# Optimization experiments

Hardware: AMD Instinct MI355X
Metric: run time of the kernel (lower is better)

## Reference

```python
import jax, jax.numpy as jnp
import numpy as np

T, C, H, E, TOPK = 8192, 1024, 4096, 8, 2
ALPHA = 0.01


def setup_inputs() -> dict:
    key = jax.random.key(0)
    ks = jax.random.split(key, 10)
    std = 0.01
    return {
        "x": jax.random.normal(ks[0], (T, C), dtype=jnp.float32),
        "gate_w": jax.random.normal(ks[1], (E, C), dtype=jnp.float32) * std,  # nn.init.normal_(std=0.01)
        "wg": jax.random.normal(ks[2], (E, C, H), dtype=jnp.float32) * 0.02,
        "wu": jax.random.normal(ks[3], (E, C, H), dtype=jnp.float32) * 0.02,
        "wd": jax.random.normal(ks[4], (E, H, C), dtype=jnp.float32) * 0.02,
        "swg": jax.random.normal(ks[5], (C, H), dtype=jnp.float32) * 0.02,
        "swu": jax.random.normal(ks[6], (C, H), dtype=jnp.float32) * 0.02,
        "swd": jax.random.normal(ks[7], (H, C), dtype=jnp.float32) * 0.02,
        "shared_scale": jnp.ones((1,), dtype=jnp.float32) * 0.5,
    }


def _swiglu(h, g, u, d):
    # SwiGLU FFN: W_down( silu(W_gate x) * W_up x )
    return (jax.nn.silu(h @ g) * (h @ u)) @ d


def reference(x, gate_w, wg, wu, wd, swg, swu, swd, shared_scale):
    # ---- gate (top-k softmax routing) ----
    logits = x @ gate_w.T                       # [T, E]
    scores = jax.nn.softmax(logits, axis=-1)    # [T, E]
    topk_w, topk_idx = jax.lax.top_k(scores, TOPK)
    topk_w = topk_w / jnp.sum(topk_w, axis=-1, keepdims=True)

    # per-token combine weight for each expert: sum_k w_k * [idx_k == e]  -> [T, E]
    comb = jnp.zeros((x.shape[0], E), dtype=x.dtype)
    comb = comb.at[jnp.arange(x.shape[0])[:, None], topk_idx].add(topk_w)

    # ---- routed experts (dispatch-FFN-combine, expressed as masked dense combine) ----
    y = jnp.zeros_like(x)
    for e in range(E):  # fixed small expert count
        y = y + comb[:, e:e + 1] * _swiglu(x, wg[e], wu[e], wd[e])

    # ---- shared expert ----
    y = y + shared_scale * _swiglu(x, swg, swu, swd)

    # ---- load-balancing aux loss (training mode) ----
    onehot = jax.nn.one_hot(topk_idx.reshape(-1), E, dtype=x.dtype)  # [T*K, E]
    ce = onehot.mean(axis=0)
    fi = ce * E
    Pi = scores.mean(axis=0)
    aux_loss = jnp.sum(Pi * fi) * ALPHA
    return y, aux_loss
```

## Files before the change

kernel.cpp:

```cpp
#include <hip/hip_runtime.h>
#include <hip/hip_bf16.h>
#include <stdint.h>

#define T_TOK 8192
#define CDIM  1024
#define HDIM  4096
#define NEXP  8
#define TOPK_ 2
#define GT_MAX 72
#define UT_MAX 104
#define GROWS_MAX (GT_MAX * 256)

typedef __attribute__((ext_vector_type(8))) short short8;
typedef __attribute__((ext_vector_type(4))) float f32x4;

__device__ __forceinline__ void gload16(const short* g, short* l) {
  __builtin_amdgcn_global_load_lds(
      (const __attribute__((address_space(1))) unsigned int*)(g),
      (__attribute__((address_space(3))) unsigned int*)(l), 16, 0, 0);
}

__global__ __launch_bounds__(256) void gate_kernel(
    const float* __restrict__ x, const float* __restrict__ gw,
    int* __restrict__ tokinfo, float* __restrict__ tokw,
    int* __restrict__ bcnt, float* __restrict__ spart,
    __hip_bfloat16* __restrict__ xb)
{
  const int wid = threadIdx.x >> 6, lane = threadIdx.x & 63;
  const int t = blockIdx.x * 4 + wid;
  float acc[NEXP];
#pragma unroll
  for (int e = 0; e < NEXP; ++e) acc[e] = 0.f;
  const float4* xr = (const float4*)x + (size_t)t * (CDIM / 4);
  const float4* gw4 = (const float4*)gw;
  uint2* xbo = (uint2*)(xb + (size_t)t * CDIM);
#pragma unroll
  for (int i = 0; i < CDIM / 256; ++i) {
    const float4 xv = xr[lane + 64 * i];
    union { __hip_bfloat16 h[4]; uint2 u; } o;
    o.h[0] = __float2bfloat16(xv.x); o.h[1] = __float2bfloat16(xv.y);
    o.h[2] = __float2bfloat16(xv.z); o.h[3] = __float2bfloat16(xv.w);
    xbo[lane + 64 * i] = o.u;
#pragma unroll
    for (int e = 0; e < NEXP; ++e) {
      const float4 gv = gw4[e * (CDIM / 4) + lane + 64 * i];
      acc[e] += xv.x * gv.x + xv.y * gv.y + xv.z * gv.z + xv.w * gv.w;
    }
  }
#pragma unroll
  for (int off = 32; off > 0; off >>= 1) {
#pragma unroll
    for (int e = 0; e < NEXP; ++e) acc[e] += __shfl_xor(acc[e], off);
  }
  float mx = acc[0];
#pragma unroll
  for (int e = 1; e < NEXP; ++e) mx = fmaxf(mx, acc[e]);
  float p[NEXP]; float s = 0.f;
#pragma unroll
  for (int e = 0; e < NEXP; ++e) { p[e] = __expf(acc[e] - mx); s += p[e]; }
  const float inv = 1.f / s;
#pragma unroll
  for (int e = 0; e < NEXP; ++e) p[e] *= inv;
  float v0 = p[0]; int i0 = 0;
#pragma unroll
  for (int e = 1; e < NEXP; ++e) if (p[e] > v0) { v0 = p[e]; i0 = e; }
  float v1 = -1.f; int i1 = 0;
#pragma unroll
  for (int e = 0; e < NEXP; ++e) if (e != i0 && p[e] > v1) { v1 = p[e]; i1 = e; }

  __shared__ float sp[4][NEXP];
  __shared__ int   se[4][2];
  __shared__ float swt[4][2];
  if (lane == 0) {
#pragma unroll
    for (int e = 0; e < NEXP; ++e) sp[wid][e] = p[e];
    const float wn = 1.f / (v0 + v1);
    se[wid][0] = i0; se[wid][1] = i1;
    swt[wid][0] = v0 * wn; swt[wid][1] = v1 * wn;
  }
  __syncthreads();
  if (threadIdx.x == 0) {
    int cnt[NEXP];
#pragma unroll
    for (int e = 0; e < NEXP; ++e) cnt[e] = 0;
#pragma unroll
    for (int tt = 0; tt < 4; ++tt) {
      const int e0 = se[tt][0], e1 = se[tt][1];
      const int r0 = cnt[e0]++; const int r1 = cnt[e1]++;
      tokinfo[blockIdx.x * 4 + tt] = e0 | (e1 << 3) | (r0 << 6) | (r1 << 10);
      ((float2*)tokw)[blockIdx.x * 4 + tt] = make_float2(swt[tt][0], swt[tt][1]);
    }
#pragma unroll
    for (int e = 0; e < NEXP; ++e) bcnt[blockIdx.x * NEXP + e] = cnt[e];
  }
  if (threadIdx.x < NEXP)
    spart[blockIdx.x * NEXP + threadIdx.x] =
        sp[0][threadIdx.x] + sp[1][threadIdx.x] + sp[2][threadIdx.x] + sp[3][threadIdx.x];
}

__global__ __launch_bounds__(512) void scan_kernel(
    const int* __restrict__ bcnt, int* __restrict__ boff, int* __restrict__ ecnt,
    const float* __restrict__ spart, float* __restrict__ aux_out,
    int* __restrict__ pad_off, int* __restrict__ tile_map, int* __restrict__ ntiles)
{
  const int w = threadIdx.x >> 6, l = threadIdx.x & 63;
  int run = 0;
#pragma unroll 4
  for (int c = 0; c < (T_TOK / 4) / 64; ++c) {
    const int b = c * 64 + l;
    const int v = bcnt[b * NEXP + w];
    int sc = v;
#pragma unroll
    for (int off = 1; off < 64; off <<= 1) {
      const int t = __shfl_up(sc, off);
      if (l >= off) sc += t;
    }
    boff[b * NEXP + w] = run + sc - v;
    run += __shfl(sc, 63);
  }
  if (l == 0) ecnt[w] = run;
  float fs = 0.f;
  for (int c = 0; c < (T_TOK / 4) / 64; ++c) fs += spart[(c * 64 + l) * NEXP + w];
#pragma unroll
  for (int off = 32; off > 0; off >>= 1) fs += __shfl_xor(fs, off);
  __shared__ float pis[NEXP];
  __shared__ int cs[NEXP];
  if (l == 0) { pis[w] = fs; cs[w] = run; }
  __syncthreads();
  if (threadIdx.x == 0) {
    float aux = 0.f;
#pragma unroll
    for (int e = 0; e < NEXP; ++e) {
      const float Pi = pis[e] / (float)T_TOK;
      const float ce = (float)cs[e] / (float)(T_TOK * TOPK_);
      aux += Pi * ce * (float)NEXP;
    }
    aux_out[0] = aux * 0.01f;
    ecnt[8] = T_TOK;
    int acc = 0, nt = 0;
    for (int e = 0; e < NEXP; ++e) {
      pad_off[e] = acc;
      const int te = (cs[e] + 255) >> 8;
      for (int t = 0; t < te; ++t) { tile_map[nt] = e | ((t * 256) << 4); ++nt; }
      acc += te * 256;
    }
    ntiles[0] = nt;
    for (int t = 0; t < T_TOK / 256; ++t) { tile_map[nt] = 8 | ((t * 256) << 4); ++nt; }
    ntiles[1] = nt;
  }
}

__global__ __launch_bounds__(256) void scatter_kernel(
    const int* __restrict__ tokinfo, const float* __restrict__ tokw,
    const int* __restrict__ boff, const int* __restrict__ pad_off,
    int* __restrict__ grows, float* __restrict__ gww, int2* __restrict__ tokpos)
{
  const int t = blockIdx.x * 256 + threadIdx.x;
  const int info = tokinfo[t];
  const int e0 = info & 7, e1 = (info >> 3) & 7;
  const int r0 = (info >> 6) & 15, r1 = (info >> 10) & 15;
  const int b = t >> 2;
  const float2 wv = ((const float2*)tokw)[t];
  const int g0 = pad_off[e0] + boff[b * NEXP + e0] + r0;
  grows[g0] = t; gww[g0] = wv.x;
  const int g1 = pad_off[e1] + boff[b * NEXP + e1] + r1;
  grows[g1] = t; gww[g1] = wv.y;
  tokpos[t] = make_int2(g0, g1);
}

struct TD { const float* src; __hip_bfloat16* dst; int N; int nsh; int M; };
struct TB { TD d[27]; };
__global__ __launch_bounds__(256) void tbatch_kernel(TB tb)
{
  const int m = blockIdx.x >> 12;
  const int t = blockIdx.x & 4095;
  const TD td = tb.d[m];
  const int n0 = (t & ((1 << td.nsh) - 1)) << 5;
  const int m0 = (t >> td.nsh) << 5;
  __shared__ float tile[32][33];
  const int tx = threadIdx.x & 31, ty = threadIdx.x >> 5;
#pragma unroll
  for (int i = 0; i < 4; ++i)
    tile[ty + 8 * i][tx] = td.src[(size_t)(m0 + ty + 8 * i) * td.N + n0 + tx];
  __syncthreads();
#pragma unroll
  for (int i = 0; i < 4; ++i)
    td.dst[(size_t)(n0 + ty + 8 * i) * td.M + m0 + tx] = __float2bfloat16(tile[tx][ty + 8 * i]);
}

__global__ __launch_bounds__(1024, 4) void gemm1_pipe_kernel(
    const __hip_bfloat16* __restrict__ Abase,
    const __hip_bfloat16* __restrict__ B0mat, const __hip_bfloat16* __restrict__ B1mat,
    __hip_bfloat16* __restrict__ midout,
    const int* __restrict__ rowlist, const int* __restrict__ ecnt,
    const int* __restrict__ tile_map, const int* __restrict__ ntiles,
    int mode, int tile_base)
{
  constexpr int K = CDIM;
  constexpr int NTL = K / 64;
  __shared__ __align__(16) short lds[65536];

  int ti = (int)blockIdx.y + tile_base;
  if (mode == 2) ti += ntiles[0];
  const int hi = (mode == 1) ? ntiles[0] : ntiles[1];
  if (ti >= hi) return;
  const int tm = tile_map[ti];
  const int e = tm & 15, rb = tm >> 4;
  const int rows_valid = ecnt[e] - rb;
  const int gbmid = (int)blockIdx.y * 256;
  const int glist = ti * 256;

  const int t = threadIdx.x, l = t & 63, w = t >> 6;
  const int wr = w >> 2, wc = w & 3;
  const int n0h = (int)blockIdx.x * 128;

  const int srow = t >> 3;
  const int ksrc = ((t & 7) ^ ((t >> 3) & 7)) * 8;
  const short* pA[2]; const short* pB[2];
#pragma unroll
  for (int j = 0; j < 2; ++j) {
    const int rl_ = j * 128 + srow;
    int rg;
    if (e == 8) rg = rb + rl_;
    else { const int c = rl_ < rows_valid ? rl_ : rows_valid - 1; rg = rowlist[glist + c]; }
    pA[j] = (const short*)Abase + (size_t)rg * K + ksrc;
    const int s = (rl_ >> 4) & 1;
    const int h = n0h + (rl_ >> 5) * 16 + (rl_ & 15);
    pB[j] = (const short*)(s ? B1mat : B0mat) + (size_t)e * CDIM * HDIM + (size_t)h * K + ksrc;
  }
  const int dst0 = t * 8;

#define STG(tt) { const int b_ = ((tt) & 1) * 16384; \
    gload16(pA[0] + (tt) * 64, lds + b_ + dst0); \
    gload16(pA[1] + (tt) * 64, lds + b_ + 8192 + dst0); \
    gload16(pB[0] + (tt) * 64, lds + 32768 + b_ + dst0); \
    gload16(pB[1] + (tt) * 64, lds + 32768 + b_ + 8192 + dst0); }

  const int l15 = l & 15;
  const int j0 = ((l >> 4) ^ (l & 7)) * 8;
  const int j1 = ((4 + (l >> 4)) ^ (l & 7)) * 8;
  const int arow = (wr * 64 + l15) * 64;
  const int brow = (wc * 64 + l15) * 64;

  f32x4 acc[4][4];
#pragma unroll
  for (int i = 0; i < 4; ++i)
#pragma unroll
    for (int j = 0; j < 4; ++j) acc[i][j] = (f32x4){0.f, 0.f, 0.f, 0.f};

  short8 af[4], bf[4];

  STG(0)
  for (int tt = 0; tt < NTL; ++tt) {
    asm volatile("s_waitcnt vmcnt(0)\n\ts_barrier" ::: "memory");
    __builtin_amdgcn_sched_barrier(0);
    if (tt + 1 < NTL) STG(tt + 1)
    const int ab = (tt & 1) * 16384, bb = 32768 + (tt & 1) * 16384;
#pragma unroll
    for (int ks = 0; ks < 2; ++ks) {
      const int cj = ks ? j1 : j0;
#pragma unroll
      for (int mi = 0; mi < 4; ++mi) af[mi] = *(const short8*)(lds + ab + arow + mi * 1024 + cj);
#pragma unroll
      for (int ni = 0; ni < 4; ++ni) bf[ni] = *(const short8*)(lds + bb + brow + ni * 1024 + cj);
      __builtin_amdgcn_s_setprio(1);
#pragma unroll
      for (int mi = 0; mi < 4; ++mi)
#pragma unroll
        for (int ni = 0; ni < 4; ++ni)
          acc[mi][ni] = __builtin_amdgcn_mfma_f32_16x16x32_bf16(af[mi], bf[ni], acc[mi][ni], 0, 0, 0);
      __builtin_amdgcn_s_setprio(0);
    }
  }
#undef STG

  const int rl = (l >> 4) * 4, cl = l & 15;
#pragma unroll
  for (int mi = 0; mi < 4; ++mi) {
#pragma unroll
    for (int j = 0; j < 4; ++j) {
      const int rlocal = wr * 64 + mi * 16 + rl + j;
      if (rlocal < rows_valid) {
        __hip_bfloat16* mp = midout + (size_t)(gbmid + rlocal) * HDIM;
#pragma unroll
        for (int jj = 0; jj < 2; ++jj) {
          const float g = acc[mi][jj * 2][j], u = acc[mi][jj * 2 + 1][j];
          const float sv = g / (1.f + __expf(-g));
          mp[n0h + wc * 32 + jj * 16 + cl] = __float2bfloat16(sv * u);
        }
      }
    }
  }
}

template <int OST>
__global__ __launch_bounds__(1024, 4) void gemm2_pipe_kernel(
    const __hip_bfloat16* __restrict__ mid, const __hip_bfloat16* __restrict__ wd9,
    float* __restrict__ mid2, float* __restrict__ y,
    const int* __restrict__ rowlist, const float* __restrict__ roww,
    const int* __restrict__ ecnt, const int* __restrict__ tile_map,
    const int* __restrict__ ntiles, const float* __restrict__ ssc,
    int mode, int tile_base)
{
  constexpr int K = HDIM;
  constexpr int NTL = K / 64;
  __shared__ __align__(16) short lds[49152];

  int ti = (int)blockIdx.y + tile_base;
  if (mode == 2) ti += ntiles[0];
  const int hi = (mode == 1) ? ntiles[0] : ntiles[1];
  if (ti >= hi) return;
  const int tm = tile_map[ti];
  const int e = tm & 15, rb = tm >> 4;
  const int rows_valid = ecnt[e] - rb;
  const int gbmid = (int)blockIdx.y * 256;
  const int glist = ti * 256;

  const int t = threadIdx.x, l = t & 63, w = t >> 6;
  const int wr = w >> 2, wc = w & 3;
  const int n0 = (int)blockIdx.x * 128;

  const int srow = t >> 3;
  const int ksrc = ((t & 7) ^ ((t >> 3) & 7)) * 8;
  const short* pA[2];
#pragma unroll
  for (int j = 0; j < 2; ++j)
    pA[j] = (const short*)mid + (size_t)(gbmid + j * 128 + srow) * K + ksrc;
  const short* pB0 = (const short*)wd9 + (size_t)e * CDIM * HDIM + (size_t)(n0 + srow) * K + ksrc;
  const int dst0 = t * 8;

#define STG2(tt) { const int a_ = ((tt) & 1) * 16384, b_ = 32768 + ((tt) & 1) * 8192; \
    gload16(pA[0] + (size_t)(tt) * 64, lds + a_ + dst0); \
    gload16(pA[1] + (size_t)(tt) * 64, lds + a_ + 8192 + dst0); \
    gload16(pB0   + (size_t)(tt) * 64, lds + b_ + dst0); }

  const int l15 = l & 15;
  const int j0 = ((l >> 4) ^ (l & 7)) * 8;
  const int j1 = ((4 + (l >> 4)) ^ (l & 7)) * 8;
  const int arow = (wr * 64 + l15) * 64;
  const int brow = (wc * 32 + l15) * 64;

  f32x4 acc[4][2];
#pragma unroll
  for (int i = 0; i < 4; ++i) { acc[i][0] = (f32x4){0.f,0.f,0.f,0.f}; acc[i][1] = (f32x4){0.f,0.f,0.f,0.f}; }

  short8 af[4], bf[2];

  STG2(0)
  for (int tt = 0; tt < NTL; ++tt) {
    asm volatile("s_waitcnt vmcnt(0)\n\ts_barrier" ::: "memory");
    __builtin_amdgcn_sched_barrier(0);
    if (tt + 1 < NTL) STG2(tt + 1)
    const int ab = (tt & 1) * 16384, bb = 32768 + (tt & 1) * 8192;
#pragma unroll
    for (int ks = 0; ks < 2; ++ks) {
      const int cj = ks ? j1 : j0;
#pragma unroll
      for (int mi = 0; mi < 4; ++mi) af[mi] = *(const short8*)(lds + ab + arow + mi * 1024 + cj);
      bf[0] = *(const short8*)(lds + bb + brow + cj);
      bf[1] = *(const short8*)(lds + bb + brow + 1024 + cj);
      __builtin_amdgcn_s_setprio(1);
#pragma unroll
      for (int mi = 0; mi < 4; ++mi) {
        acc[mi][0] = __builtin_amdgcn_mfma_f32_16x16x32_bf16(af[mi], bf[0], acc[mi][0], 0, 0, 0);
        acc[mi][1] = __builtin_amdgcn_mfma_f32_16x16x32_bf16(af[mi], bf[1], acc[mi][1], 0, 0, 0);
      }
      __builtin_amdgcn_s_setprio(0);
    }
  }
#undef STG2

  const int rl = (l >> 4) * 4, cl = l & 15;
  if (OST) {
#pragma unroll
    for (int mi = 0; mi < 4; ++mi) {
#pragma unroll
      for (int j = 0; j < 4; ++j) {
        const int rlocal = wr * 64 + mi * 16 + rl + j;
        if (rlocal < rows_valid) {
          float* mp = mid2 + (size_t)(glist + rlocal) * CDIM + n0 + wc * 32 + cl;
          mp[0]  = acc[mi][0][j];
          mp[16] = acc[mi][1][j];
        }
      }
    }
  } else {
    const float ss = ssc[0];
#pragma unroll
    for (int mi = 0; mi < 4; ++mi) {
#pragma unroll
      for (int j = 0; j < 4; ++j) {
        const int rlocal = wr * 64 + mi * 16 + rl + j;
        if (rlocal < rows_valid) {
          int tok; float wgt;
          if (e == 8) { tok = rb + rlocal; wgt = ss; }
          else { tok = rowlist[glist + rlocal]; wgt = roww[glist + rlocal]; }
          float* yp = y + (size_t)tok * CDIM + n0 + wc * 32 + cl;
          unsafeAtomicAdd(yp,      wgt * acc[mi][0][j]);
          unsafeAtomicAdd(yp + 16, wgt * acc[mi][1][j]);
        }
      }
    }
  }
}

__global__ __launch_bounds__(256) void combine_kernel(
    const float* __restrict__ mid2, const int* __restrict__ ntiles,
    const int2* __restrict__ tokpos, const float* __restrict__ tokw,
    const float* __restrict__ ssc, float* __restrict__ y)
{
  const int t = blockIdx.x;
  const int c = threadIdx.x * 4;
  const int dbase = ntiles[0] * 256;
  const int2 gp = tokpos[t];
  const float2 wv = ((const float2*)tokw)[t];
  const float ss = ssc[0];
  const float4 d = *(const float4*)(mid2 + (size_t)(dbase + t) * CDIM + c);
  const float4 a = *(const float4*)(mid2 + (size_t)gp.x * CDIM + c);
  const float4 b = *(const float4*)(mid2 + (size_t)gp.y * CDIM + c);
  float4 r;
  r.x = ss * d.x + wv.x * a.x + wv.y * b.x;
  r.y = ss * d.y + wv.x * a.y + wv.y * b.y;
  r.z = ss * d.z + wv.x * a.z + wv.y * b.z;
  r.w = ss * d.w + wv.x * a.w + wv.y * b.w;
  *(float4*)(y + (size_t)t * CDIM + c) = r;
}

extern "C" void kernel_launch(void* const* d_in, const int* in_sizes, int n_in,
                              void* d_out, int out_size, void* d_ws, size_t ws_size,
                              hipStream_t stream)
{
  const float* x   = (const float*)d_in[0];
  const float* gw  = (const float*)d_in[1];
  const float* wg  = (const float*)d_in[2];
  const float* wu  = (const float*)d_in[3];
  const float* wd  = (const float*)d_in[4];
  const float* swg = (const float*)d_in[5];
  const float* swu = (const float*)d_in[6];
  const float* swd = (const float*)d_in[7];
  const float* ssc = (const float*)d_in[8];
  float* y = (float*)d_out;

  auto al = [](size_t v) { return (v + 255) & ~(size_t)255; };
  char* ws = (char*)d_ws;
  size_t off = 0;
  __hip_bfloat16* xb = (__hip_bfloat16*)(ws + off); off += al((size_t)T_TOK * CDIM * 2);
  int*   tokinfo = (int*)(ws + off);   off += al((size_t)T_TOK * 4);
  float* tokw    = (float*)(ws + off); off += al((size_t)T_TOK * 8);
  int2*  tokpos  = (int2*)(ws + off);  off += al((size_t)T_TOK * 8);
  int*   bcnt    = (int*)(ws + off);   off += al((size_t)(T_TOK / 4) * NEXP * 4);
  int*   boffb   = (int*)(ws + off);   off += al((size_t)(T_TOK / 4) * NEXP * 4);
  float* spart   = (float*)(ws + off); off += al((size_t)(T_TOK / 4) * NEXP * 4);
  int*   ecnt    = (int*)(ws + off);   off += 256;
  int*   pad_off = (int*)(ws + off);   off += 256;
  int*   ntiles  = (int*)(ws + off);   off += 256;
  int*   tile_map= (int*)(ws + off);   off += al((size_t)UT_MAX * 4);
  int*   grows   = (int*)(ws + off);   off += al((size_t)GROWS_MAX * 4);
  float* gww     = (float*)(ws + off); off += al((size_t)GROWS_MAX * 4);

  const size_t WMAT = (size_t)CDIM * HDIM;
  __hip_bfloat16* wg9 = (__hip_bfloat16*)(ws + off); off += 9 * WMAT * 2;
  __hip_bfloat16* wu9 = (__hip_bfloat16*)(ws + off); off += 9 * WMAT * 2;
  __hip_bfloat16* wd9 = (__hip_bfloat16*)(ws + off); off += 9 * WMAT * 2;
  __hip_bfloat16* mid = (__hip_bfloat16*)(ws + off);
  const size_t mid_avail = (ws_size > off) ? (ws_size - off) : 0;
  const size_t TILE_B = (size_t)256 * HDIM * 2;
  const size_t MIDB   = (size_t)UT_MAX * TILE_B;
  const size_t MID2B  = (size_t)UT_MAX * 256 * CDIM * 4;

  gate_kernel<<<T_TOK / 4, 256, 0, stream>>>(x, gw, tokinfo, tokw, bcnt, spart, xb);
  scan_kernel<<<1, 512, 0, stream>>>(bcnt, boffb, ecnt, spart, y + (size_t)T_TOK * CDIM,
                                     pad_off, tile_map, ntiles);
  scatter_kernel<<<T_TOK / 256, 256, 0, stream>>>(tokinfo, tokw, boffb, pad_off,
                                                  grows, gww, tokpos);

  TB tb;
  for (int e = 0; e < 8; ++e) {
    tb.d[e]      = TD{wg + e * WMAT, wg9 + e * WMAT, HDIM, 7, CDIM};
    tb.d[8 + e]  = TD{wu + e * WMAT, wu9 + e * WMAT, HDIM, 7, CDIM};
    tb.d[16 + e] = TD{wd + e * WMAT, wd9 + e * WMAT, CDIM, 5, HDIM};
  }
  tb.d[24] = TD{swg, wg9 + 8 * WMAT, HDIM, 7, CDIM};
  tb.d[25] = TD{swu, wu9 + 8 * WMAT, HDIM, 7, CDIM};
  tb.d[26] = TD{swd, wd9 + 8 * WMAT, CDIM, 5, HDIM};
  tbatch_kernel<<<27 * 4096, 256, 0, stream>>>(tb);

  if (mid_avail >= MIDB + MID2B) {
    float* mid2 = (float*)((char*)mid + MIDB);
    gemm1_pipe_kernel<<<dim3(HDIM / 128, UT_MAX), 1024, 0, stream>>>(
        xb, wg9, wu9, mid, grows, ecnt, tile_map, ntiles, 0, 0);
    gemm2_pipe_kernel<1><<<dim3(CDIM / 128, UT_MAX), 1024, 0, stream>>>(
        mid, wd9, mid2, nullptr, grows, gww, ecnt, tile_map, ntiles, ssc, 0, 0);
    combine_kernel<<<T_TOK, 256, 0, stream>>>(mid2, ntiles, tokpos, tokw, ssc, y);
  } else if (mid_avail >= MIDB) {
    hipMemsetAsync(y, 0, (size_t)T_TOK * CDIM * sizeof(float), stream);
    gemm1_pipe_kernel<<<dim3(HDIM / 128, UT_MAX), 1024, 0, stream>>>(
        xb, wg9, wu9, mid, grows, ecnt, tile_map, ntiles, 0, 0);
    gemm2_pipe_kernel<0><<<dim3(CDIM / 128, UT_MAX), 1024, 0, stream>>>(
        mid, wd9, nullptr, y, grows, gww, ecnt, tile_map, ntiles, ssc, 0, 0);
  } else {
    hipMemsetAsync(y, 0, (size_t)T_TOK * CDIM * sizeof(float), stream);
    int CH = (int)(mid_avail / TILE_B);
    if (CH < 1) CH = 1;
    for (int c0 = 0; c0 < GT_MAX; c0 += CH) {
      const int g = (GT_MAX - c0) < CH ? (GT_MAX - c0) : CH;
      gemm1_pipe_kernel<<<dim3(HDIM / 128, g), 1024, 0, stream>>>(
          xb, wg9, wu9, mid, grows, ecnt, tile_map, ntiles, 1, c0);
      gemm2_pipe_kernel<0><<<dim3(CDIM / 128, g), 1024, 0, stream>>>(
          mid, wd9, nullptr, y, grows, gww, ecnt, tile_map, ntiles, ssc, 1, c0);
    }
    for (int c0 = 0; c0 < 32; c0 += CH) {
      const int g = (32 - c0) < CH ? (32 - c0) : CH;
      gemm1_pipe_kernel<<<dim3(HDIM / 128, g), 1024, 0, stream>>>(
          xb, wg9, wu9, mid, grows, ecnt, tile_map, ntiles, 2, c0);
      gemm2_pipe_kernel<0><<<dim3(CDIM / 128, g), 1024, 0, stream>>>(
          mid, wd9, nullptr, y, grows, gww, ecnt, tile_map, ntiles, ssc, 2, c0);
    }
  }
}
```

Before: 1.014 ms.

## Restructure down-projection GEMM to 512 threads with split-phase staged pipeline

The down-projection GEMM drops from 1024 to 512 threads per block. Each wave now computes a 128x32 output tile (8x2 MFMA accumulators) instead of 64x32. The K-loop splits each tile step into two A-half phases, and the next tile's A halves and B are staged at different points so the global-to-LDS loads overlap with MFMA work. Barriers and lgkmcnt waits are placed explicitly. The aim is more work per wave and better load/compute overlap, at the cost of more registers per thread and lower occupancy.

```diff
diff --git a/kernel.cpp b/kernel.cpp
--- a/kernel.cpp
+++ b/kernel.cpp
@@ -19,6 +19,10 @@
       (const __attribute__((address_space(1))) unsigned int*)(g),
       (__attribute__((address_space(3))) unsigned int*)(l), 16, 0, 0);
 }
+
+#define BAR       asm volatile("s_barrier" ::: "memory")
+#define LGKM0     do { asm volatile("s_waitcnt lgkmcnt(0)" ::: "memory"); \
+                       __builtin_amdgcn_sched_barrier(0); } while (0)
 
 __global__ __launch_bounds__(256) void gate_kernel(
     const float* __restrict__ x, const float* __restrict__ gw,
@@ -294,7 +298,7 @@
 }
 
 template <int OST>
-__global__ __launch_bounds__(1024, 4) void gemm2_pipe_kernel(
+__global__ __launch_bounds__(512, 1) void gemm2_pipe_kernel(
     const __hip_bfloat16* __restrict__ mid, const __hip_bfloat16* __restrict__ wd9,
     float* __restrict__ mid2, float* __restrict__ y,
     const int* __restrict__ rowlist, const float* __restrict__ roww,
@@ -320,63 +324,97 @@
   const int wr = w >> 2, wc = w & 3;
   const int n0 = (int)blockIdx.x * 128;
 
-  const int srow = t >> 3;
-  const int ksrc = ((t & 7) ^ ((t >> 3) & 7)) * 8;
-  const short* pA[2];
+  const int rbase = w * 8 + (l >> 3);
+  const int ksrc = ((l & 7) ^ ((l >> 3) & 7)) * 8;
+  const short* pA[4]; const short* pB[2];
+#pragma unroll
+  for (int j = 0; j < 4; ++j)
+    pA[j] = (const short*)mid + (size_t)(gbmid + j * 64 + rbase) * K + ksrc;
 #pragma unroll
   for (int j = 0; j < 2; ++j)
-    pA[j] = (const short*)mid + (size_t)(gbmid + j * 128 + srow) * K + ksrc;
-  const short* pB0 = (const short*)wd9 + (size_t)e * CDIM * HDIM + (size_t)(n0 + srow) * K + ksrc;
-  const int dst0 = t * 8;
-
-#define STG2(tt) { const int a_ = ((tt) & 1) * 16384, b_ = 32768 + ((tt) & 1) * 8192; \
-    gload16(pA[0] + (size_t)(tt) * 64, lds + a_ + dst0); \
-    gload16(pA[1] + (size_t)(tt) * 64, lds + a_ + 8192 + dst0); \
-    gload16(pB0   + (size_t)(tt) * 64, lds + b_ + dst0); }
+    pB[j] = (const short*)wd9 + (size_t)e * CDIM * HDIM + (size_t)(n0 + j * 64 + rbase) * K + ksrc;
+  const int dst0 = w * 512 + l * 8;
+
+#define STG2_AH(tt, h) { const int b_ = ((tt) & 1) * 16384; \
+    gload16(pA[2*(h)]   + (size_t)(tt) * 64, lds + b_ + (2*(h)) * 4096   + dst0); \
+    gload16(pA[2*(h)+1] + (size_t)(tt) * 64, lds + b_ + (2*(h)+1) * 4096 + dst0); }
+#define STG2_B(tt) { const int b_ = 32768 + ((tt) & 1) * 8192; \
+    gload16(pB[0] + (size_t)(tt) * 64, lds + b_ + dst0); \
+    gload16(pB[1] + (size_t)(tt) * 64, lds + b_ + 4096 + dst0); }
 
   const int l15 = l & 15;
-  const int j0 = ((l >> 4) ^ (l & 7)) * 8;
-  const int j1 = ((4 + (l >> 4)) ^ (l & 7)) * 8;
-  const int arow = (wr * 64 + l15) * 64;
-  const int brow = (wc * 32 + l15) * 64;
-
-  f32x4 acc[4][2];
-#pragma unroll
-  for (int i = 0; i < 4; ++i) { acc[i][0] = (f32x4){0.f,0.f,0.f,0.f}; acc[i][1] = (f32x4){0.f,0.f,0.f,0.f}; }
-
-  short8 af[4], bf[2];
-
-  STG2(0)
+  const int cs0 = (((l >> 4)) ^ (l & 7)) * 8;
+  const int cs1 = ((4 + (l >> 4)) ^ (l & 7)) * 8;
+  const int afb = (wr * 128 + l15) * 64;
+  const int bfb = (wc * 32 + l15) * 64;
+
+  f32x4 acc[8][2];
+#pragma unroll
+  for (int i = 0; i < 8; ++i) { acc[i][0] = (f32x4){0.f,0.f,0.f,0.f}; acc[i][1] = (f32x4){0.f,0.f,0.f,0.f}; }
+
+  short8 af[4][2], bf[2][2];
+
+  STG2_AH(0, 0) STG2_AH(0, 1) STG2_B(0)
+
   for (int tt = 0; tt < NTL; ++tt) {
-    asm volatile("s_waitcnt vmcnt(0)\n\ts_barrier" ::: "memory");
+    const int ab = (tt & 1) * 16384, bb = 32768 + (tt & 1) * 8192;
+    if (tt + 1 < NTL) {
+      STG2_AH(tt + 1, 0)
+      asm volatile("s_waitcnt vmcnt(2)\n\ts_barrier" ::: "memory");
+    } else {
+      asm volatile("s_waitcnt vmcnt(0)\n\ts_barrier" ::: "memory");
+    }
     __builtin_amdgcn_sched_barrier(0);
-    if (tt + 1 < NTL) STG2(tt + 1)
-    const int ab = (tt & 1) * 16384, bb = 32768 + (tt & 1) * 8192;
-#pragma unroll
-    for (int ks = 0; ks < 2; ++ks) {
-      const int cj = ks ? j1 : j0;
-#pragma unroll
-      for (int mi = 0; mi < 4; ++mi) af[mi] = *(const short8*)(lds + ab + arow + mi * 1024 + cj);
-      bf[0] = *(const short8*)(lds + bb + brow + cj);
-      bf[1] = *(const short8*)(lds + bb + brow + 1024 + cj);
-      __builtin_amdgcn_s_setprio(1);
-#pragma unroll
-      for (int mi = 0; mi < 4; ++mi) {
-        acc[mi][0] = __builtin_amdgcn_mfma_f32_16x16x32_bf16(af[mi], bf[0], acc[mi][0], 0, 0, 0);
-        acc[mi][1] = __builtin_amdgcn_mfma_f32_16x16x32_bf16(af[mi], bf[1], acc[mi][1], 0, 0, 0);
-      }
-      __builtin_amdgcn_s_setprio(0);
-    }
-  }
-#undef STG2
+#pragma unroll
+    for (int mi = 0; mi < 4; ++mi) {
+      af[mi][0] = *(const short8*)(lds + ab + afb + mi * 1024 + cs0);
+      af[mi][1] = *(const short8*)(lds + ab + afb + mi * 1024 + cs1);
+    }
+#pragma unroll
+    for (int ni = 0; ni < 2; ++ni) {
+      bf[ni][0] = *(const short8*)(lds + bb + bfb + ni * 1024 + cs0);
+      bf[ni][1] = *(const short8*)(lds + bb + bfb + ni * 1024 + cs1);
+    }
+    if (tt + 1 < NTL) STG2_AH(tt + 1, 1)
+    BAR; LGKM0;
+    __builtin_amdgcn_s_setprio(1);
+#pragma unroll
+    for (int ks = 0; ks < 2; ++ks)
+#pragma unroll
+      for (int mi = 0; mi < 4; ++mi)
+#pragma unroll
+        for (int ni = 0; ni < 2; ++ni)
+          acc[mi][ni] = __builtin_amdgcn_mfma_f32_16x16x32_bf16(af[mi][ks], bf[ni][ks], acc[mi][ni], 0, 0, 0);
+    __builtin_amdgcn_s_setprio(0);
+    BAR;
+#pragma unroll
+    for (int mi = 0; mi < 4; ++mi) {
+      af[mi][0] = *(const short8*)(lds + ab + afb + 4096 + mi * 1024 + cs0);
+      af[mi][1] = *(const short8*)(lds + ab + afb + 4096 + mi * 1024 + cs1);
+    }
+    if (tt + 1 < NTL) STG2_B(tt + 1)
+    BAR; LGKM0;
+    __builtin_amdgcn_s_setprio(1);
+#pragma unroll
+    for (int ks = 0; ks < 2; ++ks)
+#pragma unroll
+      for (int mi = 0; mi < 4; ++mi)
+#pragma unroll
+        for (int ni = 0; ni < 2; ++ni)
+          acc[4 + mi][ni] = __builtin_amdgcn_mfma_f32_16x16x32_bf16(af[mi][ks], bf[ni][ks], acc[4 + mi][ni], 0, 0, 0);
+    __builtin_amdgcn_s_setprio(0);
+    BAR;
+  }
+#undef STG2_AH
+#undef STG2_B
 
   const int rl = (l >> 4) * 4, cl = l & 15;
   if (OST) {
 #pragma unroll
-    for (int mi = 0; mi < 4; ++mi) {
+    for (int mi = 0; mi < 8; ++mi) {
 #pragma unroll
       for (int j = 0; j < 4; ++j) {
-        const int rlocal = wr * 64 + mi * 16 + rl + j;
+        const int rlocal = wr * 128 + mi * 16 + rl + j;
         if (rlocal < rows_valid) {
           float* mp = mid2 + (size_t)(glist + rlocal) * CDIM + n0 + wc * 32 + cl;
           mp[0]  = acc[mi][0][j];
@@ -387,10 +425,10 @@
   } else {
     const float ss = ssc[0];
 #pragma unroll
-    for (int mi = 0; mi < 4; ++mi) {
+    for (int mi = 0; mi < 8; ++mi) {
 #pragma unroll
       for (int j = 0; j < 4; ++j) {
-        const int rlocal = wr * 64 + mi * 16 + rl + j;
+        const int rlocal = wr * 128 + mi * 16 + rl + j;
         if (rlocal < rows_valid) {
           int tok; float wgt;
           if (e == 8) { tok = rb + rlocal; wgt = ss; }
@@ -489,14 +527,14 @@
     float* mid2 = (float*)((char*)mid + MIDB);
     gemm1_pipe_kernel<<<dim3(HDIM / 128, UT_MAX), 1024, 0, stream>>>(
         xb, wg9, wu9, mid, grows, ecnt, tile_map, ntiles, 0, 0);
-    gemm2_pipe_kernel<1><<<dim3(CDIM / 128, UT_MAX), 1024, 0, stream>>>(
+    gemm2_pipe_kernel<1><<<dim3(CDIM / 128, UT_MAX), 512, 0, stream>>>(
         mid, wd9, mid2, nullptr, grows, gww, ecnt, tile_map, ntiles, ssc, 0, 0);
     combine_kernel<<<T_TOK, 256, 0, stream>>>(mid2, ntiles, tokpos, tokw, ssc, y);
   } else if (mid_avail >= MIDB) {
     hipMemsetAsync(y, 0, (size_t)T_TOK * CDIM * sizeof(float), stream);
     gemm1_pipe_kernel<<<dim3(HDIM / 128, UT_MAX), 1024, 0, stream>>>(
         xb, wg9, wu9, mid, grows, ecnt, tile_map, ntiles, 0, 0);
-    gemm2_pipe_kernel<0><<<dim3(CDIM / 128, UT_MAX), 1024, 0, stream>>>(
+    gemm2_pipe_kernel<0><<<dim3(CDIM / 128, UT_MAX), 512, 0, stream>>>(
         mid, wd9, nullptr, y, grows, gww, ecnt, tile_map, ntiles, ssc, 0, 0);
   } else {
     hipMemsetAsync(y, 0, (size_t)T_TOK * CDIM * sizeof(float), stream);
@@ -506,14 +544,14 @@
       const int g = (GT_MAX - c0) < CH ? (GT_MAX - c0) : CH;
       gemm1_pipe_kernel<<<dim3(HDIM / 128, g), 1024, 0, stream>>>(
           xb, wg9, wu9, mid, grows, ecnt, tile_map, ntiles, 1, c0);
-      gemm2_pipe_kernel<0><<<dim3(CDIM / 128, g), 1024, 0, stream>>>(
+      gemm2_pipe_kernel<0><<<dim3(CDIM / 128, g), 512, 0, stream>>>(
           mid, wd9, nullptr, y, grows, gww, ecnt, tile_map, ntiles, ssc, 1, c0);
     }
     for (int c0 = 0; c0 < 32; c0 += CH) {
       const int g = (32 - c0) < CH ? (32 - c0) : CH;
       gemm1_pipe_kernel<<<dim3(HDIM / 128, g), 1024, 0, stream>>>(
           xb, wg9, wu9, mid, grows, ecnt, tile_map, ntiles, 2, c0);
-      gemm2_pipe_kernel<0><<<dim3(CDIM / 128, g), 1024, 0, stream>>>(
+      gemm2_pipe_kernel<0><<<dim3(CDIM / 128, g), 512, 0, stream>>>(
           mid, wd9, nullptr, y, grows, gww, ecnt, tile_map, ntiles, ssc, 2, c0);
     }
   }
```

New measurement: 982.8 us, median of 2. -3.0%, faster.
